# Optimization experiments

Hardware: AMD Instinct MI355X
Metric: run time of the kernel (lower is better)

The kernel has to match this reference:

```python
import jax, jax.numpy as jnp
import numpy as np

FP8_E4M3_MAX = 448.0  # max representable magnitude of float8_e4m3fn

def fake_quant_fp8(t):
    """Per-tensor dynamic-scale fp8 (e4m3) quantize + dequantize."""
    amax = jnp.max(jnp.abs(t))
    scale = FP8_E4M3_MAX / jnp.maximum(amax, 1e-12)
    q = (t * scale).astype(jnp.float8_e4m3fn).astype(jnp.float32)
    return q / scale

def setup_inputs() -> dict:
    key = jax.random.key(0)
    k1, k2, k3 = jax.random.split(key, 3)
    d_in, d_out = 1024, 1024
    x = jax.random.normal(k1, (4, 8192, d_in), dtype=jnp.float32)
    weight = jax.random.normal(k2, (d_out, d_in), dtype=jnp.float32) * (1.0 / np.sqrt(d_in))
    bias = jax.random.normal(k3, (d_out,), dtype=jnp.float32) * 0.01
    return {"x": x, "weight": weight, "bias": bias}

def reference(x, weight, bias):
    # fp8-quantized linear: quantize activations and weights to e4m3 with
    # per-tensor dynamic scales, matmul, dequant (folded into fake-quant), add bias.
    xq = fake_quant_fp8(x)        # [b, s, d_in]
    wq = fake_quant_fp8(weight)   # [d_out, d_in]
    return jnp.einsum('bsd,od->bso', xq, wq) + bias
```

## Files before the change

### kernel.cpp

```cpp
#include <hip/hip_runtime.h>
#include <stdint.h>

typedef float floatx4 __attribute__((ext_vector_type(4)));
typedef int intx8 __attribute__((ext_vector_type(8)));

#define FP8_MAX 448.0f
#define BM 128
#define BN 128
#define BK 128
#define GX 2048
#define GW 256

__global__ void amax_partial(const float* __restrict__ x, long n4x,
                             const float* __restrict__ w, long n4w,
                             float* __restrict__ part) {
    const float4* p4; long n4, i0, stride;
    if (blockIdx.x < GX) {
        p4 = (const float4*)x; n4 = n4x;
        i0 = (long)blockIdx.x * blockDim.x + threadIdx.x;
        stride = (long)GX * blockDim.x;
    } else {
        p4 = (const float4*)w; n4 = n4w;
        i0 = (long)(blockIdx.x - GX) * blockDim.x + threadIdx.x;
        stride = (long)GW * blockDim.x;
    }
    float m = 0.f;
    for (long i = i0; i < n4; i += stride) {
        float4 v = p4[i];
        m = fmaxf(m, fmaxf(fmaxf(fabsf(v.x), fabsf(v.y)),
                           fmaxf(fabsf(v.z), fabsf(v.w))));
    }
    #pragma unroll
    for (int off = 32; off > 0; off >>= 1) m = fmaxf(m, __shfl_down(m, off, 64));
    __shared__ float red[4];
    if ((threadIdx.x & 63) == 0) red[threadIdx.x >> 6] = m;
    __syncthreads();
    if (threadIdx.x == 0)
        part[blockIdx.x] = fmaxf(fmaxf(red[0], red[1]), fmaxf(red[2], red[3]));
}

__global__ void finalize_scales(const float* __restrict__ part, float* __restrict__ scales) {
    float mx = 0.f, mw = 0.f;
    for (int i = threadIdx.x; i < GX; i += 256) mx = fmaxf(mx, part[i]);
    for (int i = GX + threadIdx.x; i < GX + GW; i += 256) mw = fmaxf(mw, part[i]);
    #pragma unroll
    for (int off = 32; off > 0; off >>= 1) {
        mx = fmaxf(mx, __shfl_down(mx, off, 64));
        mw = fmaxf(mw, __shfl_down(mw, off, 64));
    }
    __shared__ float rx[4], rw[4];
    if ((threadIdx.x & 63) == 0) { rx[threadIdx.x >> 6] = mx; rw[threadIdx.x >> 6] = mw; }
    __syncthreads();
    if (threadIdx.x == 0) {
        float ax = fmaxf(fmaxf(rx[0], rx[1]), fmaxf(rx[2], rx[3]));
        float aw = fmaxf(fmaxf(rw[0], rw[1]), fmaxf(rw[2], rw[3]));
        float sx = FP8_MAX / fmaxf(ax, 1e-12f);
        float sw = FP8_MAX / fmaxf(aw, 1e-12f);
        scales[0] = sx; scales[1] = sw; scales[2] = 1.0f / (sx * sw);
    }
}

__global__ void quant_kernel(const float* __restrict__ x, int4* __restrict__ xq, long n16x,
                             const float* __restrict__ w, int4* __restrict__ wq, long n16w,
                             const float* __restrict__ scales) {
    const float4* p4; int4* o; long n16, i0, stride; float s;
    if (blockIdx.x < GX) {
        p4 = (const float4*)x; o = xq; n16 = n16x; s = scales[0];
        i0 = (long)blockIdx.x * blockDim.x + threadIdx.x;
        stride = (long)GX * blockDim.x;
    } else {
        p4 = (const float4*)w; o = wq; n16 = n16w; s = scales[1];
        i0 = (long)(blockIdx.x - GX) * blockDim.x + threadIdx.x;
        stride = (long)GW * blockDim.x;
    }
    for (long i = i0; i < n16; i += stride) {
        float4 v0 = p4[i * 4 + 0];
        float4 v1 = p4[i * 4 + 1];
        float4 v2 = p4[i * 4 + 2];
        float4 v3 = p4[i * 4 + 3];
        int w0 = 0, w1 = 0, w2 = 0, w3 = 0;
        w0 = __builtin_amdgcn_cvt_pk_fp8_f32(v0.x * s, v0.y * s, w0, false);
        w0 = __builtin_amdgcn_cvt_pk_fp8_f32(v0.z * s, v0.w * s, w0, true);
        w1 = __builtin_amdgcn_cvt_pk_fp8_f32(v1.x * s, v1.y * s, w1, false);
        w1 = __builtin_amdgcn_cvt_pk_fp8_f32(v1.z * s, v1.w * s, w1, true);
        w2 = __builtin_amdgcn_cvt_pk_fp8_f32(v2.x * s, v2.y * s, w2, false);
        w2 = __builtin_amdgcn_cvt_pk_fp8_f32(v2.z * s, v2.w * s, w2, true);
        w3 = __builtin_amdgcn_cvt_pk_fp8_f32(v3.x * s, v3.y * s, w3, false);
        w3 = __builtin_amdgcn_cvt_pk_fp8_f32(v3.z * s, v3.w * s, w3, true);
        o[i] = make_int4(w0, w1, w2, w3);
    }
}

__global__ __launch_bounds__(256) void gemm_fp8mx(
    const unsigned char* __restrict__ Aq, const unsigned char* __restrict__ Bq,
    const float* __restrict__ bias, const float* __restrict__ scales,
    float* __restrict__ out, int M, int N, int K) {
    __shared__ __align__(16) unsigned char tA[BM * BK];
    __shared__ __align__(16) unsigned char tB[BN * BK];

    const int tid = threadIdx.x;
    const int lane = tid & 63;
    const int wave = tid >> 6;
    const int waveM = (wave & 1) * 64;
    const int waveN = (wave >> 1) * 64;

    const int nbx = gridDim.x;
    const int nwg = nbx * gridDim.y;
    int bx = blockIdx.x, by = blockIdx.y;
    if (nbx == 8 && (nwg & 7) == 0) {
        const int f   = by * 8 + bx;
        const int per = nwg >> 3;
        const int sw  = (f & 7) * per + (f >> 3);
        bx = sw & 7;
        by = sw >> 3;
    }
    const long m0 = (long)by * BM;
    const int n0 = bx * BN;

    const int srow = lane >> 3;
    const int sphys = lane & 7;

    floatx4 acc[4][4];
    #pragma unroll
    for (int i = 0; i < 4; ++i)
        #pragma unroll
        for (int j = 0; j < 4; ++j)
            acc[i][j] = (floatx4){0.f, 0.f, 0.f, 0.f};

    const int row16 = lane & 15;
    const int q2 = (lane >> 4) * 2;

    for (int k0 = 0; k0 < K; k0 += BK) {
        __syncthreads();
        #pragma unroll
        for (int c = 0; c < 4; ++c) {
            const int r = wave * 32 + c * 8 + srow;
            const int lc = (sphys ^ (r & 7)) * 16;
            __builtin_amdgcn_global_load_lds(
                (const __attribute__((address_space(1))) void*)(Aq + (m0 + r) * (long)K + k0 + lc),
                (__attribute__((address_space(3))) void*)&tA[r * BK + sphys * 16], 16, 0, 0);
            __builtin_amdgcn_global_load_lds(
                (const __attribute__((address_space(1))) void*)(Bq + (long)(n0 + r) * K + k0 + lc),
                (__attribute__((address_space(3))) void*)&tB[r * BK + sphys * 16], 16, 0, 0);
        }
        __syncthreads();

        intx8 af[4], bf[4];
        #pragma unroll
        for (int t = 0; t < 4; ++t) {
            const int row = waveM + t * 16 + row16;
            const int s = row & 7;
            const int4 lo = *(const int4*)&tA[row * BK + ((q2 ^ s)) * 16];
            const int4 hi = *(const int4*)&tA[row * BK + (((q2 + 1) ^ s)) * 16];
            af[t] = (intx8){lo.x, lo.y, lo.z, lo.w, hi.x, hi.y, hi.z, hi.w};
        }
        #pragma unroll
        for (int t = 0; t < 4; ++t) {
            const int row = waveN + t * 16 + row16;
            const int s = row & 7;
            const int4 lo = *(const int4*)&tB[row * BK + ((q2 ^ s)) * 16];
            const int4 hi = *(const int4*)&tB[row * BK + (((q2 + 1) ^ s)) * 16];
            bf[t] = (intx8){lo.x, lo.y, lo.z, lo.w, hi.x, hi.y, hi.z, hi.w};
        }
        #pragma unroll
        for (int mt = 0; mt < 4; ++mt)
            #pragma unroll
            for (int nt = 0; nt < 4; ++nt)
                acc[mt][nt] = __builtin_amdgcn_mfma_scale_f32_16x16x128_f8f6f4(
                    af[mt], bf[nt], acc[mt][nt], 0, 0,
                    0, 127, 0, 127);
    }

    const float inv = scales[2];
    const int col = lane & 15;
    const int rbase4 = (lane >> 4) * 4;
    #pragma unroll
    for (int nt = 0; nt < 4; ++nt) {
        const int gn = n0 + waveN + nt * 16 + col;
        const float bv = bias[gn];
        #pragma unroll
        for (int mt = 0; mt < 4; ++mt) {
            const long gm = m0 + waveM + mt * 16 + rbase4;
            float* po = out + gm * (long)N + gn;
            #pragma unroll
            for (int r = 0; r < 4; ++r)
                po[(long)r * N] = acc[mt][nt][r] * inv + bv;
        }
    }
}

extern "C" void kernel_launch(void* const* d_in, const int* in_sizes, int n_in,
                              void* d_out, int out_size, void* d_ws, size_t ws_size,
                              hipStream_t stream) {
    const float* x = (const float*)d_in[0];
    const float* w = (const float*)d_in[1];
    const float* bias = (const float*)d_in[2];
    float* out = (float*)d_out;

    const long nx = in_sizes[0];
    const long nw = in_sizes[1];
    const int N = in_sizes[2];
    const long K = nw / N;
    const long M = nx / K;

    unsigned char* ws = (unsigned char*)d_ws;
    unsigned char* xq = ws;
    unsigned char* wq = ws + nx;
    float* part = (float*)(ws + nx + nw);
    float* scales = (float*)(ws + nx + nw + 16384);

    amax_partial<<<GX + GW, 256, 0, stream>>>(x, nx / 4, w, nw / 4, part);
    finalize_scales<<<1, 256, 0, stream>>>(part, scales);
    quant_kernel<<<GX + GW, 256, 0, stream>>>(x, (int4*)xq, nx / 16,
                                              w, (int4*)wq, nw / 16, scales);

    dim3 grid(N / BN, (int)(M / BM));
    gemm_fp8mx<<<grid, 256, 0, stream>>>(xq, wq, bias, scales, out,
                                         (int)M, N, (int)K);
}
```

Measured before the change: 297.3 us.

## Fuse scale finalize into quant kernel and double-buffer GEMM LDS tiles

Removes the single-block finalize_scales launch: every quant block now reduces the amax partials itself and derives the scales, and block 0 writes them for the GEMM epilogue. The GEMM moves to two LDS buffers, so the global-to-LDS load of the next K tile is issued before the current tile is computed, using an explicit vmcnt wait and raw barriers. Output stores become nontemporal. The cost is a redundant partial reduction in every quant block, twice the LDS per workgroup (possibly lower occupancy), a redundant reload of the last tile on the final iteration, and a hand-tuned vmcnt count that must match the number of loads issued.

Measured after the change: 292.4 us. About the same (-1.6%).

```diff
diff --git a/kernel.cpp b/kernel.cpp
--- a/kernel.cpp
+++ b/kernel.cpp
@@ -39,39 +39,39 @@
         part[blockIdx.x] = fmaxf(fmaxf(red[0], red[1]), fmaxf(red[2], red[3]));
 }
 
-__global__ void finalize_scales(const float* __restrict__ part, float* __restrict__ scales) {
+__global__ void quant_all(const float* __restrict__ part,
+                          const float* __restrict__ x, int4* __restrict__ xq, long n16x,
+                          const float* __restrict__ w, int4* __restrict__ wq, long n16w,
+                          float* __restrict__ scales) {
+    const int tid = threadIdx.x;
     float mx = 0.f, mw = 0.f;
-    for (int i = threadIdx.x; i < GX; i += 256) mx = fmaxf(mx, part[i]);
-    for (int i = GX + threadIdx.x; i < GX + GW; i += 256) mw = fmaxf(mw, part[i]);
+    for (int i = tid; i < GX; i += 256) mx = fmaxf(mx, part[i]);
+    for (int i = GX + tid; i < GX + GW; i += 256) mw = fmaxf(mw, part[i]);
     #pragma unroll
     for (int off = 32; off > 0; off >>= 1) {
         mx = fmaxf(mx, __shfl_down(mx, off, 64));
         mw = fmaxf(mw, __shfl_down(mw, off, 64));
     }
     __shared__ float rx[4], rw[4];
-    if ((threadIdx.x & 63) == 0) { rx[threadIdx.x >> 6] = mx; rw[threadIdx.x >> 6] = mw; }
+    if ((tid & 63) == 0) { rx[tid >> 6] = mx; rw[tid >> 6] = mw; }
     __syncthreads();
-    if (threadIdx.x == 0) {
-        float ax = fmaxf(fmaxf(rx[0], rx[1]), fmaxf(rx[2], rx[3]));
-        float aw = fmaxf(fmaxf(rw[0], rw[1]), fmaxf(rw[2], rw[3]));
-        float sx = FP8_MAX / fmaxf(ax, 1e-12f);
-        float sw = FP8_MAX / fmaxf(aw, 1e-12f);
+    const float ax = fmaxf(fmaxf(rx[0], rx[1]), fmaxf(rx[2], rx[3]));
+    const float aw = fmaxf(fmaxf(rw[0], rw[1]), fmaxf(rw[2], rw[3]));
+    const float sx = FP8_MAX / fmaxf(ax, 1e-12f);
+    const float sw = FP8_MAX / fmaxf(aw, 1e-12f);
+    if (blockIdx.x == 0 && tid == 0) {
         scales[0] = sx; scales[1] = sw; scales[2] = 1.0f / (sx * sw);
     }
-}
-
-__global__ void quant_kernel(const float* __restrict__ x, int4* __restrict__ xq, long n16x,
-                             const float* __restrict__ w, int4* __restrict__ wq, long n16w,
-                             const float* __restrict__ scales) {
+
     const float4* p4; int4* o; long n16, i0, stride; float s;
     if (blockIdx.x < GX) {
-        p4 = (const float4*)x; o = xq; n16 = n16x; s = scales[0];
-        i0 = (long)blockIdx.x * blockDim.x + threadIdx.x;
-        stride = (long)GX * blockDim.x;
+        p4 = (const float4*)x; o = xq; n16 = n16x; s = sx;
+        i0 = (long)blockIdx.x * 256 + tid;
+        stride = (long)GX * 256;
     } else {
-        p4 = (const float4*)w; o = wq; n16 = n16w; s = scales[1];
-        i0 = (long)(blockIdx.x - GX) * blockDim.x + threadIdx.x;
-        stride = (long)GW * blockDim.x;
+        p4 = (const float4*)w; o = wq; n16 = n16w; s = sw;
+        i0 = (long)(blockIdx.x - GX) * 256 + tid;
+        stride = (long)GW * 256;
     }
     for (long i = i0; i < n16; i += stride) {
         float4 v0 = p4[i * 4 + 0];
@@ -95,8 +95,8 @@
     const unsigned char* __restrict__ Aq, const unsigned char* __restrict__ Bq,
     const float* __restrict__ bias, const float* __restrict__ scales,
     float* __restrict__ out, int M, int N, int K) {
-    __shared__ __align__(16) unsigned char tA[BM * BK];
-    __shared__ __align__(16) unsigned char tB[BN * BK];
+    __shared__ __align__(16) unsigned char tA[2][BM * BK];
+    __shared__ __align__(16) unsigned char tB[2][BN * BK];
 
     const int tid = threadIdx.x;
     const int lane = tid & 63;
@@ -130,37 +130,51 @@
     const int row16 = lane & 15;
     const int q2 = (lane >> 4) * 2;
 
-    for (int k0 = 0; k0 < K; k0 += BK) {
-        __syncthreads();
-        #pragma unroll
-        for (int c = 0; c < 4; ++c) {
-            const int r = wave * 32 + c * 8 + srow;
-            const int lc = (sphys ^ (r & 7)) * 16;
-            __builtin_amdgcn_global_load_lds(
-                (const __attribute__((address_space(1))) void*)(Aq + (m0 + r) * (long)K + k0 + lc),
-                (__attribute__((address_space(3))) void*)&tA[r * BK + sphys * 16], 16, 0, 0);
-            __builtin_amdgcn_global_load_lds(
-                (const __attribute__((address_space(1))) void*)(Bq + (long)(n0 + r) * K + k0 + lc),
-                (__attribute__((address_space(3))) void*)&tB[r * BK + sphys * 16], 16, 0, 0);
+#define STAGE(kt, b) do {                                                            \
+    const int kb_ = (kt);                                                            \
+    _Pragma("unroll")                                                                \
+    for (int c = 0; c < 4; ++c) {                                                    \
+        const int r_ = wave * 32 + c * 8 + srow;                                     \
+        const int lc_ = (sphys ^ (r_ & 7)) * 16;     \
+        __builtin_amdgcn_global_load_lds(                                            \
+            (const __attribute__((address_space(1))) void*)(Aq + (m0 + r_) * (long)K + kb_ + lc_), \
+            (__attribute__((address_space(3))) void*)&tA[b][r_ * BK + sphys * 16], 16, 0, 0);      \
+        __builtin_amdgcn_global_load_lds(                                            \
+            (const __attribute__((address_space(1))) void*)(Bq + (long)(n0 + r_) * K + kb_ + lc_), \
+            (__attribute__((address_space(3))) void*)&tB[b][r_ * BK + sphys * 16], 16, 0, 0);      \
+    } } while (0)
+
+    const int NT = K / BK;
+    const int KLAST = K - BK;
+
+    STAGE(0, 0);
+
+    for (int t = 0; t < NT; ++t) {
+        const int cur = t & 1;
+        const int nxt = cur ^ 1;
+        const int kst = (t + 1 < NT) ? (t + 1) * BK : KLAST;
+        STAGE(kst, nxt);
+
+        asm volatile("s_waitcnt vmcnt(8)" ::: "memory");
+        __builtin_amdgcn_s_barrier();
+        __builtin_amdgcn_sched_barrier(0);
+
+        intx8 af[4], bf[4];
+        #pragma unroll
+        for (int u = 0; u < 4; ++u) {
+            const int row = waveM + u * 16 + row16;
+            const int s = row & 7;
+            const int4 lo = *(const int4*)&tA[cur][row * BK + ((q2 ^ s)) * 16];
+            const int4 hi = *(const int4*)&tA[cur][row * BK + (((q2 + 1) ^ s)) * 16];
+            af[u] = (intx8){lo.x, lo.y, lo.z, lo.w, hi.x, hi.y, hi.z, hi.w};
         }
-        __syncthreads();
-
-        intx8 af[4], bf[4];
-        #pragma unroll
-        for (int t = 0; t < 4; ++t) {
-            const int row = waveM + t * 16 + row16;
+        #pragma unroll
+        for (int u = 0; u < 4; ++u) {
+            const int row = waveN + u * 16 + row16;
             const int s = row & 7;
-            const int4 lo = *(const int4*)&tA[row * BK + ((q2 ^ s)) * 16];
-            const int4 hi = *(const int4*)&tA[row * BK + (((q2 + 1) ^ s)) * 16];
-            af[t] = (intx8){lo.x, lo.y, lo.z, lo.w, hi.x, hi.y, hi.z, hi.w};
-        }
-        #pragma unroll
-        for (int t = 0; t < 4; ++t) {
-            const int row = waveN + t * 16 + row16;
-            const int s = row & 7;
-            const int4 lo = *(const int4*)&tB[row * BK + ((q2 ^ s)) * 16];
-            const int4 hi = *(const int4*)&tB[row * BK + (((q2 + 1) ^ s)) * 16];
-            bf[t] = (intx8){lo.x, lo.y, lo.z, lo.w, hi.x, hi.y, hi.z, hi.w};
+            const int4 lo = *(const int4*)&tB[cur][row * BK + ((q2 ^ s)) * 16];
+            const int4 hi = *(const int4*)&tB[cur][row * BK + (((q2 + 1) ^ s)) * 16];
+            bf[u] = (intx8){lo.x, lo.y, lo.z, lo.w, hi.x, hi.y, hi.z, hi.w};
         }
         #pragma unroll
         for (int mt = 0; mt < 4; ++mt)
@@ -169,7 +183,11 @@
                 acc[mt][nt] = __builtin_amdgcn_mfma_scale_f32_16x16x128_f8f6f4(
                     af[mt], bf[nt], acc[mt][nt], 0, 0,
                     0, 127, 0, 127);
-    }
+
+        __builtin_amdgcn_s_barrier();
+        __builtin_amdgcn_sched_barrier(0);
+    }
+#undef STAGE
 
     const float inv = scales[2];
     const int col = lane & 15;
@@ -184,7 +202,7 @@
             float* po = out + gm * (long)N + gn;
             #pragma unroll
             for (int r = 0; r < 4; ++r)
-                po[(long)r * N] = acc[mt][nt][r] * inv + bv;
+                __builtin_nontemporal_store(acc[mt][nt][r] * inv + bv, po + (long)r * N);
         }
     }
 }
@@ -210,9 +228,8 @@
     float* scales = (float*)(ws + nx + nw + 16384);
 
     amax_partial<<<GX + GW, 256, 0, stream>>>(x, nx / 4, w, nw / 4, part);
-    finalize_scales<<<1, 256, 0, stream>>>(part, scales);
-    quant_kernel<<<GX + GW, 256, 0, stream>>>(x, (int4*)xq, nx / 16,
-                                              w, (int4*)wq, nw / 16, scales);
+    quant_all<<<GX + GW, 256, 0, stream>>>(part, x, (int4*)xq, nx / 16,
+                                           w, (int4*)wq, nw / 16, scales);
 
     dim3 grid(N / BN, (int)(M / BM));
     gemm_fp8mx<<<grid, 256, 0, stream>>>(xq, wq, bias, scales, out,
```
